# Performance work log

Measured on AMD Instinct MI355X. Metric: run time of the kernel, lower is better.

The kernel has to match this reference:

```python
import jax, jax.numpy as jnp
import numpy as np
from jax import lax

B, CX, CZ, H, W = 8, 96, 96, 256, 256
HEADS = 4


def conv2d(x, w, groups=1, pad=0):
    return lax.conv_general_dilated(
        x, w, window_strides=(1, 1), padding=[(pad, pad), (pad, pad)],
        dimension_numbers=('NCHW', 'OIHW', 'NCHW'),
        feature_group_count=groups)


def setup_inputs() -> dict:
    key = jax.random.key(0)
    ks = jax.random.split(key, 8)
    def init_w(k, shape):
        fan_in = shape[1] * shape[2] * shape[3]
        bound = 1.0 / np.sqrt(fan_in)
        return jax.random.uniform(k, shape, jnp.float32, -bound, bound)
    return {
        'x': jax.random.normal(ks[0], (B, CX, H, W), jnp.float32),
        'z': jax.random.normal(ks[1], (B, CZ, H, W), jnp.float32),
        'kv_w1': init_w(ks[2], (2 * CZ, CZ, 1, 1)),
        'kv_w2': init_w(ks[3], (2 * CZ, 2, 3, 3)),   # grouped: groups=CZ, 2 in-ch per group
        'q_w1': init_w(ks[4], (CX, CX, 1, 1)),
        'q_w2': init_w(ks[5], (CX, 1, 3, 3)),        # depthwise: groups=CX
        'proj_w': init_w(ks[6], (CX, CX, 1, 1)),
        'temperature': jnp.ones((HEADS, 1, 1), jnp.float32),
    }


def _forward(x, z, kv_w1, kv_w2, q_w1, q_w2, proj_w, temperature):
    b, cx, h, w = x.shape
    cz = z.shape[1]
    hw = h * w
    kv = conv2d(conv2d(z, kv_w1), kv_w2, groups=cz, pad=1)   # [b, 2cz, h, w]
    q = conv2d(conv2d(x, q_w1), q_w2, groups=cx, pad=1)      # [b, cx, h, w]
    k, v = jnp.split(kv, 2, axis=1)
    # b (head c) h w -> b head c (h w)
    q = q.reshape(b, HEADS, cx // HEADS, hw)
    k = k.reshape(b, HEADS, cz // HEADS, hw)
    v = v.reshape(b, HEADS, cz // HEADS, hw)
    # L2 normalize along hw (torch F.normalize: x / max(||x||, eps))
    eps = 1e-12
    q = q / jnp.maximum(jnp.linalg.norm(q, axis=-1, keepdims=True), eps)
    k = k / jnp.maximum(jnp.linalg.norm(k, axis=-1, keepdims=True), eps)
    attn = jnp.einsum('bhcn,bhdn->bhcd', q, k) * temperature  # [b,head,cq,ck]
    attn = jax.nn.softmax(attn, axis=-1)
    out = jnp.einsum('bhcd,bhdn->bhcn', attn, v)              # [b,head,cq,hw]
    out = out.reshape(b, cx, h, w)
    return conv2d(out, proj_w)


def reference(x, z, kv_w1, kv_w2, q_w1, q_w2, proj_w, temperature):
    return _forward(x, z, kv_w1, kv_w2, q_w1, q_w2, proj_w, temperature)
```

## Files before the change

### kernel.cpp

```cpp
#include <hip/hip_runtime.h>
#include <math.h>

#define HWc 65536
#define Wd 256
#define Hd 256

typedef __attribute__((ext_vector_type(8))) short bf16x8;
typedef __attribute__((ext_vector_type(4))) float f32x4;

__device__ inline ushort f2bf_hi(float a) {
    uint u = __float_as_uint(a);
    uint r = u + 0x7FFFu + ((u >> 16) & 1u);
    return (ushort)(r >> 16);
}
__device__ inline float bf2f(ushort h) { return __uint_as_float((uint)h << 16); }

static const size_t SSQ_Q_OFF = 0;
static const size_t SSQ_K_OFF = 768;
static const size_t ATTN_OFF  = 1536;
static const size_t W2T_OFF   = 19968;
static const size_t KVW1T_OFF = 93696;
static const size_t QW1T_OFF  = 112128;
static const size_t WS1_OFF   = 121344;

__global__ void transpose_w_kernel(const float* __restrict__ w, float* __restrict__ wT,
                                   int O, int I) {
    int idx = blockIdx.x * 256 + threadIdx.x;
    if (idx < O * I) {
        int o = idx / I, c = idx % I;
        wT[(size_t)c * O + o] = w[idx];
    }
}

__global__ __launch_bounds__(384) void conv1x1_mfma(
    const float* __restrict__ in, const float* __restrict__ wT,
    int cstride, int woff, float* __restrict__ out)
{
    __shared__ ushort Ah[64][104];
    __shared__ ushort Al[64][104];
    int b = blockIdx.y;
    int px0 = blockIdx.x * 64;
    int t = threadIdx.x, lane = t & 63, wv = t >> 6;
    const float* inb = in + (size_t)b * 96 * HWc + px0;

    int m = 16 * wv + (lane & 15);
    int kbase = (lane >> 4) * 8;
    bf16x8 Bh[3], Bl[3];
#pragma unroll
    for (int ks = 0; ks < 3; ++ks) {
#pragma unroll
        for (int j = 0; j < 8; ++j) {
            int c = ks * 32 + kbase + j;
            float wval = wT[(size_t)c * cstride + woff + m];
            ushort hi = f2bf_hi(wval);
            float lo = wval - bf2f(hi);
            Bh[ks][j] = (short)hi;
            Bl[ks][j] = (short)f2bf_hi(lo);
        }
    }

#pragma unroll
    for (int rr = 0; rr < 4; ++rr) {
        int fi = rr * 384 + t;
        int c = fi >> 4;
        int p4 = (fi & 15) * 4;
        float4 v = *(const float4*)(inb + (size_t)c * HWc + p4);
        float vv[4] = {v.x, v.y, v.z, v.w};
#pragma unroll
        for (int e = 0; e < 4; ++e) {
            ushort hi = f2bf_hi(vv[e]);
            float lo = vv[e] - bf2f(hi);
            Ah[p4 + e][c] = hi;
            Al[p4 + e][c] = (ushort)f2bf_hi(lo);
        }
    }
    __syncthreads();

    f32x4 acc0 = {0.f, 0.f, 0.f, 0.f};
    f32x4 acc1 = {0.f, 0.f, 0.f, 0.f};
    f32x4 acc2 = {0.f, 0.f, 0.f, 0.f};
    f32x4 acc3 = {0.f, 0.f, 0.f, 0.f};
    int prow = lane & 15;

#pragma unroll
    for (int ks = 0; ks < 3; ++ks) {
        int ccol = ks * 32 + kbase;
#define DO_PT(PT, ACC)                                                         \
        {                                                                      \
            bf16x8 ah = *(const bf16x8*)&Ah[(PT) * 16 + prow][ccol];           \
            bf16x8 al = *(const bf16x8*)&Al[(PT) * 16 + prow][ccol];           \
            ACC = __builtin_amdgcn_mfma_f32_16x16x32_bf16(ah, Bh[ks], ACC, 0, 0, 0); \
            ACC = __builtin_amdgcn_mfma_f32_16x16x32_bf16(ah, Bl[ks], ACC, 0, 0, 0); \
            ACC = __builtin_amdgcn_mfma_f32_16x16x32_bf16(al, Bh[ks], ACC, 0, 0, 0); \
        }
        DO_PT(0, acc0) DO_PT(1, acc1) DO_PT(2, acc2) DO_PT(3, acc3)
#undef DO_PT
    }

    int pq = (lane >> 4) * 4;
    float* outm = out + (size_t)b * 96 * HWc + (size_t)m * HWc + px0 + pq;
    *(f32x4*)(outm + 0)  = acc0;
    *(f32x4*)(outm + 16) = acc1;
    *(f32x4*)(outm + 32) = acc2;
    *(f32x4*)(outm + 48) = acc3;
}

__global__ __launch_bounds__(256) void depthwise3x3_kernel(
    const float* __restrict__ in, const float* __restrict__ wq,
    float* __restrict__ out, float* __restrict__ ssq_q)
{
    __shared__ float red[4];
    int c = blockIdx.y, b = blockIdx.z;
    int t = threadIdx.x;
    int lane = t & 63;
    int xq = lane * 4;
    int yb = blockIdx.x * 32 + (t >> 6) * 8;

    const float* inc = in + ((size_t)(b * 96 + c)) * HWc;
    float* outc = out + ((size_t)(b * 96 + c)) * HWc;

    float w[9];
    const float* wp = wq + (size_t)c * 9;
#pragma unroll
    for (int i = 0; i < 9; ++i) w[i] = wp[i];

    float rows[3][6];

#define LOAD_ROW(yy, slot)                                                     \
    {                                                                          \
        float4 v_;                                                             \
        if ((unsigned)(yy) < (unsigned)Hd)                                     \
            v_ = *(const float4*)(inc + (size_t)(yy) * Wd + xq);               \
        else                                                                   \
            v_ = make_float4(0.f, 0.f, 0.f, 0.f);                              \
        float lw_ = __shfl_up(v_.w, 1, 64);                                    \
        float rx_ = __shfl_down(v_.x, 1, 64);                                  \
        rows[slot][0] = (lane > 0) ? lw_ : 0.f;                                \
        rows[slot][1] = v_.x; rows[slot][2] = v_.y;                            \
        rows[slot][3] = v_.z; rows[slot][4] = v_.w;                            \
        rows[slot][5] = (lane < 63) ? rx_ : 0.f;                               \
    }

    LOAD_ROW(yb - 1, 0);
    LOAD_ROW(yb, 1);

    float ssq = 0.f;
#pragma unroll
    for (int r = 0; r < 8; ++r) {
        LOAD_ROW(yb + r + 1, (r + 2) % 3);
        const float* ra = rows[r % 3];
        const float* rb = rows[(r + 1) % 3];
        const float* rc = rows[(r + 2) % 3];
        float a[4] = {0.f, 0.f, 0.f, 0.f};
#pragma unroll
        for (int dx = 0; dx < 3; ++dx)
#pragma unroll
            for (int px = 0; px < 4; ++px) {
                a[px] = fmaf(w[dx],     ra[px + dx], a[px]);
                a[px] = fmaf(w[3 + dx], rb[px + dx], a[px]);
                a[px] = fmaf(w[6 + dx], rc[px + dx], a[px]);
            }
        *(float4*)(outc + (size_t)(yb + r) * Wd + xq) = *(float4*)a;
#pragma unroll
        for (int px = 0; px < 4; ++px) ssq = fmaf(a[px], a[px], ssq);
    }
#undef LOAD_ROW

#pragma unroll
    for (int off = 32; off; off >>= 1) ssq += __shfl_down(ssq, off, 64);
    int wvi = t >> 6;
    if (lane == 0) red[wvi] = ssq;
    __syncthreads();
    if (t == 0) atomicAdd(&ssq_q[b * 96 + c], red[0] + red[1] + red[2] + red[3]);
}

#define CONV_PAIR(P, SS0, SS1)                                                 \
    {                                                                          \
        const float* m0 = midb + (size_t)(2 * (P)) * HWc;                      \
        const float* m1 = m0 + HWc;                                            \
        const float* wp_ = &wls[(P) * 36];                                     \
        float k0[4] = {0.f, 0.f, 0.f, 0.f};                                    \
        float k1[4] = {0.f, 0.f, 0.f, 0.f};                                    \
        _Pragma("unroll")                                                      \
        for (int dy = 0; dy < 3; ++dy) {                                       \
            int yy = y + dy - 1;                                               \
            if ((unsigned)yy < (unsigned)Hd) {                                 \
                _Pragma("unroll")                                              \
                for (int ic = 0; ic < 2; ++ic) {                               \
                    const float* base = (ic ? m1 : m0) + (size_t)yy * Wd;      \
                    float4 cv = *(const float4*)(base + x0);                   \
                    float rr[6];                                               \
                    rr[0] = (x0 > 0) ? base[x0 - 1] : 0.f;                     \
                    rr[1] = cv.x; rr[2] = cv.y; rr[3] = cv.z; rr[4] = cv.w;    \
                    rr[5] = (x0 < 252) ? base[x0 + 4] : 0.f;                   \
                    int wb_ = ic * 9 + dy * 3;                                 \
                    _Pragma("unroll")                                          \
                    for (int px = 0; px < 4; ++px) {                           \
                        _Pragma("unroll")                                      \
                        for (int dx = 0; dx < 3; ++dx) {                       \
                            k0[px] = fmaf(wp_[wb_ + dx],      rr[px + dx], k0[px]); \
                            k1[px] = fmaf(wp_[18 + wb_ + dx], rr[px + dx], k1[px]); \
                        }                                                      \
                    }                                                          \
                }                                                              \
            }                                                                  \
        }                                                                      \
        _Pragma("unroll")                                                      \
        for (int px = 0; px < 4; ++px) {                                       \
            SS0 = fmaf(k0[px], k0[px], SS0);                                   \
            SS1 = fmaf(k1[px], k1[px], SS1);                                   \
        }                                                                      \
        *(float4*)&ks[2 * (P)][l32 * 4]     = *(float4*)k0;                    \
        *(float4*)&ks[2 * (P) + 1][l32 * 4] = *(float4*)k1;                    \
    }

__global__ __launch_bounds__(256) void k_logits_kernel(
    const float* __restrict__ mid, const float* __restrict__ w2,
    const float* __restrict__ qg, float* __restrict__ attn_raw,
    float* __restrict__ ssq_k)
{
    __shared__ float qs[24][132];
    __shared__ float ks[24][132];
    __shared__ float wls[24 * 18];

    int bx = blockIdx.x;
    int yt = bx >> 1, xh = bx & 1;
    int h = blockIdx.y, b = blockIdx.z;
    int xbase = xh * 128;
    int t = threadIdx.x, lane = t & 63, wvi = t >> 6;
    int hi = lane >> 5, l32 = lane & 31;
    int i0 = (lane >> 3) * 3, j0 = (lane & 7) * 3;

    const float* midb = mid + ((size_t)b * 96 + h * 24) * HWc;
    const float* qb   = qg  + ((size_t)b * 96 + h * 24) * HWc;

    if (t < 108)
        *(float4*)&wls[4 * t] = *(const float4*)(w2 + (size_t)h * 432 + 4 * t);

    int pA = 2 * wvi + hi;
    int pB = 8 + 2 * wvi + hi;
    int x0 = xbase + l32 * 4;

    float acc[3][3];
#pragma unroll
    for (int a = 0; a < 3; ++a)
#pragma unroll
        for (int c2 = 0; c2 < 3; ++c2) acc[a][c2] = 0.f;
    float ssqA0 = 0.f, ssqA1 = 0.f, ssqB0 = 0.f, ssqB1 = 0.f;

    __syncthreads();

    for (int r = 0; r < 8; ++r) {
        int y = yt * 8 + r;
        __syncthreads();

        {
            const float* qrow = qb + (size_t)y * Wd + xbase;
            int fi = t;
            *(float4*)&qs[fi >> 5][(fi & 31) * 4] =
                *(const float4*)(qrow + (size_t)(fi >> 5) * HWc + (fi & 31) * 4);
            fi = t + 256;
            *(float4*)&qs[fi >> 5][(fi & 31) * 4] =
                *(const float4*)(qrow + (size_t)(fi >> 5) * HWc + (fi & 31) * 4);
        }
        CONV_PAIR(pA, ssqA0, ssqA1);
        if (t < 128) {
            CONV_PAIR(pB, ssqB0, ssqB1);
        } else {
            const float* qrow = qb + (size_t)y * Wd + xbase;
            int fi = 512 + (t - 128);
            *(float4*)&qs[fi >> 5][(fi & 31) * 4] =
                *(const float4*)(qrow + (size_t)(fi >> 5) * HWc + (fi & 31) * 4);
            fi = 640 + (t - 128);
            *(float4*)&qs[fi >> 5][(fi & 31) * 4] =
                *(const float4*)(qrow + (size_t)(fi >> 5) * HWc + (fi & 31) * 4);
        }
        __syncthreads();

        int n0 = wvi * 32;
#pragma unroll 4
        for (int nn = 0; nn < 8; ++nn) {
            int n = n0 + nn * 4;
            float4 q0v = *(const float4*)&qs[i0][n];
            float4 q1v = *(const float4*)&qs[i0 + 1][n];
            float4 q2v = *(const float4*)&qs[i0 + 2][n];
            float4 k0v = *(const float4*)&ks[j0][n];
            float4 k1v = *(const float4*)&ks[j0 + 1][n];
            float4 k2v = *(const float4*)&ks[j0 + 2][n];
            acc[0][0] += q0v.x*k0v.x + q0v.y*k0v.y + q0v.z*k0v.z + q0v.w*k0v.w;
            acc[0][1] += q0v.x*k1v.x + q0v.y*k1v.y + q0v.z*k1v.z + q0v.w*k1v.w;
            acc[0][2] += q0v.x*k2v.x + q0v.y*k2v.y + q0v.z*k2v.z + q0v.w*k2v.w;
            acc[1][0] += q1v.x*k0v.x + q1v.y*k0v.y + q1v.z*k0v.z + q1v.w*k0v.w;
            acc[1][1] += q1v.x*k1v.x + q1v.y*k1v.y + q1v.z*k1v.z + q1v.w*k1v.w;
            acc[1][2] += q1v.x*k2v.x + q1v.y*k2v.y + q1v.z*k2v.z + q1v.w*k2v.w;
            acc[2][0] += q2v.x*k0v.x + q2v.y*k0v.y + q2v.z*k0v.z + q2v.w*k0v.w;
            acc[2][1] += q2v.x*k1v.x + q2v.y*k1v.y + q2v.z*k1v.z + q2v.w*k1v.w;
            acc[2][2] += q2v.x*k2v.x + q2v.y*k2v.y + q2v.z*k2v.z + q2v.w*k2v.w;
        }
    }

    {
        float s0 = ssqA0, s1 = ssqA1;
#pragma unroll
        for (int off = 16; off; off >>= 1) {
            s0 += __shfl_down(s0, off, 32);
            s1 += __shfl_down(s1, off, 32);
        }
        if (l32 == 0) {
            atomicAdd(&ssq_k[b * 96 + h * 24 + 2 * pA],     s0);
            atomicAdd(&ssq_k[b * 96 + h * 24 + 2 * pA + 1], s1);
        }
    }
    if (t < 128) {
        float s0 = ssqB0, s1 = ssqB1;
#pragma unroll
        for (int off = 16; off; off >>= 1) {
            s0 += __shfl_down(s0, off, 32);
            s1 += __shfl_down(s1, off, 32);
        }
        if (l32 == 0) {
            atomicAdd(&ssq_k[b * 96 + h * 24 + 2 * pB],     s0);
            atomicAdd(&ssq_k[b * 96 + h * 24 + 2 * pB + 1], s1);
        }
    }

    __syncthreads();
    float* redbuf = &qs[0][0];
#pragma unroll
    for (int a = 0; a < 3; ++a)
#pragma unroll
        for (int c2 = 0; c2 < 3; ++c2)
            redbuf[wvi * 576 + (i0 + a) * 24 + (j0 + c2)] = acc[a][c2];
    __syncthreads();
    for (int p_ = t; p_ < 576; p_ += 256) {
        float s4 = redbuf[p_] + redbuf[576 + p_] + redbuf[1152 + p_] + redbuf[1728 + p_];
        atomicAdd(&attn_raw[((size_t)b * 4 + h) * 576 + p_], s4);
    }
}

__global__ __launch_bounds__(256) void softmax_fold_kernel(
    const float* __restrict__ attn_raw,
    const float* __restrict__ ssq_q, const float* __restrict__ ssq_k,
    const float* __restrict__ temp, const float* __restrict__ projw,
    float* __restrict__ W2T)
{
    __shared__ float s[24][25];
    __shared__ float rq[24], rk[24];
    int h = blockIdx.x, b = blockIdx.y;
    int t = threadIdx.x;

    if (t < 24) {
        rq[t] = 1.f / fmaxf(sqrtf(ssq_q[b * 96 + h * 24 + t]), 1e-12f);
        rk[t] = 1.f / fmaxf(sqrtf(ssq_k[b * 96 + h * 24 + t]), 1e-12f);
    }
    __syncthreads();
    float T = temp[h];
    for (int p = t; p < 576; p += 256) {
        int i = p / 24, j = p % 24;
        s[i][j] = attn_raw[(size_t)(b * 4 + h) * 576 + p] * T * rq[i] * rk[j];
    }
    __syncthreads();
    if (t < 24) {
        float m = -1e30f;
#pragma unroll
        for (int j = 0; j < 24; ++j) m = fmaxf(m, s[t][j]);
        float sum = 0.f;
#pragma unroll
        for (int j = 0; j < 24; ++j) { float e = __expf(s[t][j] - m); s[t][j] = e; sum += e; }
        float inv = 1.f / sum;
#pragma unroll
        for (int j = 0; j < 24; ++j) s[t][j] *= inv;
    }
    __syncthreads();
    for (int m_ = t; m_ < 96 * 24; m_ += 256) {
        int d = m_ % 24, co = m_ / 24;
        float acc = 0.f;
#pragma unroll
        for (int c = 0; c < 24; ++c)
            acc += projw[co * 96 + h * 24 + c] * s[c][d];
        W2T[(size_t)b * 9216 + (size_t)(h * 24 + d) * 96 + co] = acc;
    }
}

__global__ __launch_bounds__(256) void v_proj_kernel(
    const float* __restrict__ mid, const float* __restrict__ w2,
    const float* __restrict__ W2T, float* __restrict__ out)
{
    __shared__ float v_lds[48][128];
    __shared__ float wls[48 * 36];

    int bx = blockIdx.x, b = blockIdx.y;
    int y0 = (bx >> 1) * 2;
    int x0 = (bx & 1) * 128;
    int t = threadIdx.x;
    const float* midb = mid + (size_t)b * 96 * HWc;

    {
        const float* vw = w2 + 96 * 18;
        for (int i = t; i < 432; i += 256)
            *(float4*)&wls[4 * i] = *(const float4*)(vw + 4 * i);
    }

    int x = t & 127;
    int mh = __builtin_amdgcn_readfirstlane(t >> 7);
    const float* wb2 = W2T + (size_t)b * 9216 + mh * 48;

    int s4 = (t & 31) * 4;
    int xg = x0 + s4;

#pragma unroll 1
    for (int r = 0; r < 2; ++r) {
        int y = y0 + r;
        float acc[48];
#pragma unroll
        for (int m = 0; m < 48; ++m) acc[m] = 0.f;

#pragma unroll 1
        for (int cc = 0; cc < 2; ++cc) {
            __syncthreads();
#pragma unroll
            for (int j = 0; j < 3; ++j) {
                int pair = cc * 24 + j * 8 + (t >> 5);
                const float* m0 = midb + (size_t)(2 * pair) * HWc;
                const float* m1 = m0 + HWc;
                const float* wp_ = &wls[pair * 36];
                float k0[4] = {0.f, 0.f, 0.f, 0.f};
                float k1[4] = {0.f, 0.f, 0.f, 0.f};
#pragma unroll
                for (int dy = 0; dy < 3; ++dy) {
                    int yy = y + dy - 1;
                    if ((unsigned)yy < (unsigned)Hd) {
#pragma unroll
                        for (int ic = 0; ic < 2; ++ic) {
                            const float* base = (ic ? m1 : m0) + (size_t)yy * Wd;
                            float4 cv = *(const float4*)(base + xg);
                            float rr[6];
                            rr[0] = (xg > 0) ? base[xg - 1] : 0.f;
                            rr[1] = cv.x; rr[2] = cv.y; rr[3] = cv.z; rr[4] = cv.w;
                            rr[5] = (xg < 252) ? base[xg + 4] : 0.f;
                            int wb_ = ic * 9 + dy * 3;
#pragma unroll
                            for (int px = 0; px < 4; ++px) {
#pragma unroll
                                for (int dx = 0; dx < 3; ++dx) {
                                    k0[px] = fmaf(wp_[wb_ + dx],      rr[px + dx], k0[px]);
                                    k1[px] = fmaf(wp_[18 + wb_ + dx], rr[px + dx], k1[px]);
                                }
                            }
                        }
                    }
                }
                int lc = 2 * (j * 8 + (t >> 5));
                *(float4*)&v_lds[lc][s4]     = *(float4*)k0;
                *(float4*)&v_lds[lc + 1][s4] = *(float4*)k1;
            }
            __syncthreads();
#pragma unroll 4
            for (int cl = 0; cl < 48; ++cl) {
                float v = v_lds[cl][x];
                const float* wc = wb2 + (size_t)(cc * 48 + cl) * 96;
#pragma unroll
                for (int m = 0; m < 48; ++m) acc[m] = fmaf(wc[m], v, acc[m]);
            }
        }

        float* outb = out + (size_t)b * 96 * HWc + (size_t)(mh * 48) * HWc
                    + (size_t)y * Wd + x0 + x;
#pragma unroll
        for (int m = 0; m < 48; ++m) outb[(size_t)m * HWc] = acc[m];
    }
}

extern "C" void kernel_launch(void* const* d_in, const int* in_sizes, int n_in,
                              void* d_out, int out_size, void* d_ws, size_t ws_size,
                              hipStream_t stream) {
    const float* x     = (const float*)d_in[0];
    const float* z     = (const float*)d_in[1];
    const float* kvw1  = (const float*)d_in[2];
    const float* kvw2  = (const float*)d_in[3];
    const float* qw1   = (const float*)d_in[4];
    const float* qw2   = (const float*)d_in[5];
    const float* projw = (const float*)d_in[6];
    const float* temp  = (const float*)d_in[7];
    float* out = (float*)d_out;
    float* ws  = (float*)d_ws;
    (void)in_sizes; (void)n_in; (void)out_size; (void)ws_size;

    float* ssq_q = ws + SSQ_Q_OFF;
    float* ssq_k = ws + SSQ_K_OFF;
    float* attn  = ws + ATTN_OFF;
    float* W2T   = ws + W2T_OFF;
    float* kvw1T = ws + KVW1T_OFF;
    float* qw1T  = ws + QW1T_OFF;
    float* ws1   = ws + WS1_OFF;

    hipMemsetAsync(ws, 0, (768 + 768 + 18432) * sizeof(float), stream);

    transpose_w_kernel<<<dim3(72), 256, 0, stream>>>(kvw1, kvw1T, 192, 96);
    transpose_w_kernel<<<dim3(36), 256, 0, stream>>>(qw1, qw1T, 96, 96);

    conv1x1_mfma<<<dim3(1024, 8), 384, 0, stream>>>(x, qw1T, 96, 0, ws1);
    depthwise3x3_kernel<<<dim3(8, 96, 8), 256, 0, stream>>>(ws1, qw2, out, ssq_q);

    conv1x1_mfma<<<dim3(1024, 8), 384, 0, stream>>>(z, kvw1T, 192, 0, ws1);
    k_logits_kernel<<<dim3(64, 4, 8), 256, 0, stream>>>(ws1, kvw2, out, attn, ssq_k);

    softmax_fold_kernel<<<dim3(4, 8), 256, 0, stream>>>(attn, ssq_q, ssq_k, temp, projw, W2T);

    conv1x1_mfma<<<dim3(1024, 8), 384, 0, stream>>>(z, kvw1T, 192, 96, ws1);
    v_proj_kernel<<<dim3(256, 8), 256, 0, stream>>>(ws1, kvw2, W2T, out);
}
```

Baseline: 777.1 us.

## Move fused V-conv and projection to split-bf16 MFMA, prepack weight fragments

The final stage, a grouped 3x3 on V followed by the folded attention-times-projection matrix, now stages the V tile into swizzled LDS as hi/lo bf16 pairs. It then does the 96x96 channel mix with bf16 MFMA using three products per pair to keep near-fp32 accuracy, replacing the scalar FMA loop over 48 register accumulators. The 1x1 conv weights and the folded W2 are pre-split into hi/lo bf16 fragments in a prep kernel, so each conv block loads vectors instead of converting weights per element. The trade-off is smaller blocks with redundant halo loads for the 3x3, plus a small precision change from the bf16 split.

```diff
diff --git a/kernel.cpp b/kernel.cpp
--- a/kernel.cpp
+++ b/kernel.cpp
@@ -18,23 +18,28 @@
 static const size_t SSQ_Q_OFF = 0;
 static const size_t SSQ_K_OFF = 768;
 static const size_t ATTN_OFF  = 1536;
-static const size_t W2T_OFF   = 19968;
-static const size_t KVW1T_OFF = 93696;
-static const size_t QW1T_OFF  = 112128;
+static const size_t QWF_OFF   = 19968;
+static const size_t KWF_OFF   = 29184;
+static const size_t VWF_OFF   = 38400;
+static const size_t W2F_OFF   = 47616;
 static const size_t WS1_OFF   = 121344;
 
-__global__ void transpose_w_kernel(const float* __restrict__ w, float* __restrict__ wT,
-                                   int O, int I) {
+__global__ void prep_wfrag(const float* __restrict__ w, int woff,
+                           ushort* __restrict__ wf) {
     int idx = blockIdx.x * 256 + threadIdx.x;
-    if (idx < O * I) {
-        int o = idx / I, c = idx % I;
-        wT[(size_t)c * O + o] = w[idx];
+    if (idx < 9216) {
+        int m = idx / 96, c = idx % 96;
+        float val = w[(size_t)(woff + m) * 96 + c];
+        ushort hi = f2bf_hi(val);
+        float lo = val - bf2f(hi);
+        wf[(c >> 5) * 3072 + m * 32 + (c & 31)] = hi;
+        wf[9216 + (c >> 5) * 3072 + m * 32 + (c & 31)] = f2bf_hi(lo);
     }
 }
 
 __global__ __launch_bounds__(384) void conv1x1_mfma(
-    const float* __restrict__ in, const float* __restrict__ wT,
-    int cstride, int woff, float* __restrict__ out)
+    const float* __restrict__ in, const ushort* __restrict__ wf,
+    float* __restrict__ out)
 {
     __shared__ ushort Ah[64][104];
     __shared__ ushort Al[64][104];
@@ -48,15 +53,8 @@
     bf16x8 Bh[3], Bl[3];
 #pragma unroll
     for (int ks = 0; ks < 3; ++ks) {
-#pragma unroll
-        for (int j = 0; j < 8; ++j) {
-            int c = ks * 32 + kbase + j;
-            float wval = wT[(size_t)c * cstride + woff + m];
-            ushort hi = f2bf_hi(wval);
-            float lo = wval - bf2f(hi);
-            Bh[ks][j] = (short)hi;
-            Bl[ks][j] = (short)f2bf_hi(lo);
-        }
+        Bh[ks] = *(const bf16x8*)&wf[ks * 3072 + m * 32 + kbase];
+        Bl[ks] = *(const bf16x8*)&wf[9216 + ks * 3072 + m * 32 + kbase];
     }
 
 #pragma unroll
@@ -342,7 +340,7 @@
     const float* __restrict__ attn_raw,
     const float* __restrict__ ssq_q, const float* __restrict__ ssq_k,
     const float* __restrict__ temp, const float* __restrict__ projw,
-    float* __restrict__ W2T)
+    ushort* __restrict__ W2F)
 {
     __shared__ float s[24][25];
     __shared__ float rq[24], rk[24];
@@ -372,103 +370,131 @@
         for (int j = 0; j < 24; ++j) s[t][j] *= inv;
     }
     __syncthreads();
+    ushort* wfb = W2F + (size_t)b * 18432;
     for (int m_ = t; m_ < 96 * 24; m_ += 256) {
         int d = m_ % 24, co = m_ / 24;
         float acc = 0.f;
 #pragma unroll
         for (int c = 0; c < 24; ++c)
             acc += projw[co * 96 + h * 24 + c] * s[c][d];
-        W2T[(size_t)b * 9216 + (size_t)(h * 24 + d) * 96 + co] = acc;
-    }
-}
-
-__global__ __launch_bounds__(256) void v_proj_kernel(
+        int dv = h * 24 + d;
+        int ks = dv >> 5, kk = dv & 31;
+        ushort hi = f2bf_hi(acc);
+        float lo = acc - bf2f(hi);
+        wfb[ks * 3072 + co * 32 + kk] = hi;
+        wfb[9216 + ks * 3072 + co * 32 + kk] = f2bf_hi(lo);
+    }
+}
+
+__global__ __launch_bounds__(384) void v_proj_mfma(
     const float* __restrict__ mid, const float* __restrict__ w2,
-    const float* __restrict__ W2T, float* __restrict__ out)
+    const ushort* __restrict__ W2F, float* __restrict__ out)
 {
-    __shared__ float v_lds[48][128];
-    __shared__ float wls[48 * 36];
+    __shared__ ushort Ah[64][128];
+    __shared__ ushort Al[64][128];
+    __shared__ float wls[1728];
 
     int bx = blockIdx.x, b = blockIdx.y;
-    int y0 = (bx >> 1) * 2;
-    int x0 = (bx & 1) * 128;
-    int t = threadIdx.x;
+    int y = bx >> 2;
+    int x0 = (bx & 3) * 64;
+    int t = threadIdx.x, lane = t & 63, wv = t >> 6;
     const float* midb = mid + (size_t)b * 96 * HWc;
 
+    for (int i = t; i < 432; i += 384)
+        *(float4*)&wls[4 * i] = *(const float4*)(w2 + 96 * 18 + 4 * i);
+
+    int m = 16 * wv + (lane & 15);
+    int kbase = (lane >> 4) * 8;
+    const ushort* wfb = W2F + (size_t)b * 18432;
+    bf16x8 Bh[3], Bl[3];
+#pragma unroll
+    for (int ks = 0; ks < 3; ++ks) {
+        Bh[ks] = *(const bf16x8*)&wfb[ks * 3072 + m * 32 + kbase];
+        Bl[ks] = *(const bf16x8*)&wfb[9216 + ks * 3072 + m * 32 + kbase];
+    }
+    __syncthreads();
+
     {
-        const float* vw = w2 + 96 * 18;
-        for (int i = t; i < 432; i += 256)
-            *(float4*)&wls[4 * i] = *(const float4*)(vw + 4 * i);
-    }
-
-    int x = t & 127;
-    int mh = __builtin_amdgcn_readfirstlane(t >> 7);
-    const float* wb2 = W2T + (size_t)b * 9216 + mh * 48;
-
-    int s4 = (t & 31) * 4;
-    int xg = x0 + s4;
-
-#pragma unroll 1
-    for (int r = 0; r < 2; ++r) {
-        int y = y0 + r;
-        float acc[48];
-#pragma unroll
-        for (int m = 0; m < 48; ++m) acc[m] = 0.f;
-
-#pragma unroll 1
-        for (int cc = 0; cc < 2; ++cc) {
-            __syncthreads();
-#pragma unroll
-            for (int j = 0; j < 3; ++j) {
-                int pair = cc * 24 + j * 8 + (t >> 5);
-                const float* m0 = midb + (size_t)(2 * pair) * HWc;
-                const float* m1 = m0 + HWc;
-                const float* wp_ = &wls[pair * 36];
-                float k0[4] = {0.f, 0.f, 0.f, 0.f};
-                float k1[4] = {0.f, 0.f, 0.f, 0.f};
-#pragma unroll
-                for (int dy = 0; dy < 3; ++dy) {
-                    int yy = y + dy - 1;
-                    if ((unsigned)yy < (unsigned)Hd) {
-#pragma unroll
-                        for (int ic = 0; ic < 2; ++ic) {
-                            const float* base = (ic ? m1 : m0) + (size_t)yy * Wd;
-                            float4 cv = *(const float4*)(base + xg);
-                            float rr[6];
-                            rr[0] = (xg > 0) ? base[xg - 1] : 0.f;
-                            rr[1] = cv.x; rr[2] = cv.y; rr[3] = cv.z; rr[4] = cv.w;
-                            rr[5] = (xg < 252) ? base[xg + 4] : 0.f;
-                            int wb_ = ic * 9 + dy * 3;
-#pragma unroll
-                            for (int px = 0; px < 4; ++px) {
-#pragma unroll
-                                for (int dx = 0; dx < 3; ++dx) {
-                                    k0[px] = fmaf(wp_[wb_ + dx],      rr[px + dx], k0[px]);
-                                    k1[px] = fmaf(wp_[18 + wb_ + dx], rr[px + dx], k1[px]);
-                                }
-                            }
+        int p = t >> 3;
+        int xl = (t & 7) * 8;
+        int xg = x0 + xl;
+        const float* m0 = midb + (size_t)(2 * p) * HWc;
+        const float* m1 = m0 + HWc;
+        const float* wp_ = &wls[p * 36];
+        float k0[8] = {0.f,0.f,0.f,0.f,0.f,0.f,0.f,0.f};
+        float k1[8] = {0.f,0.f,0.f,0.f,0.f,0.f,0.f,0.f};
+#pragma unroll
+        for (int dy = 0; dy < 3; ++dy) {
+            int yy = y + dy - 1;
+            if ((unsigned)yy < (unsigned)Hd) {
+#pragma unroll
+                for (int ic = 0; ic < 2; ++ic) {
+                    const float* base = (ic ? m1 : m0) + (size_t)yy * Wd;
+                    float4 a = *(const float4*)(base + xg);
+                    float4 b2 = *(const float4*)(base + xg + 4);
+                    float rr[10];
+                    rr[0] = (xg > 0) ? base[xg - 1] : 0.f;
+                    rr[1] = a.x; rr[2] = a.y; rr[3] = a.z; rr[4] = a.w;
+                    rr[5] = b2.x; rr[6] = b2.y; rr[7] = b2.z; rr[8] = b2.w;
+                    rr[9] = (xg + 8 < 256) ? base[xg + 8] : 0.f;
+                    int wb_ = ic * 9 + dy * 3;
+#pragma unroll
+                    for (int px = 0; px < 8; ++px) {
+#pragma unroll
+                        for (int dx = 0; dx < 3; ++dx) {
+                            k0[px] = fmaf(wp_[wb_ + dx],      rr[px + dx], k0[px]);
+                            k1[px] = fmaf(wp_[18 + wb_ + dx], rr[px + dx], k1[px]);
                         }
                     }
                 }
-                int lc = 2 * (j * 8 + (t >> 5));
-                *(float4*)&v_lds[lc][s4]     = *(float4*)k0;
-                *(float4*)&v_lds[lc + 1][s4] = *(float4*)k1;
             }
-            __syncthreads();
-#pragma unroll 4
-            for (int cl = 0; cl < 48; ++cl) {
-                float v = v_lds[cl][x];
-                const float* wc = wb2 + (size_t)(cc * 48 + cl) * 96;
-#pragma unroll
-                for (int m = 0; m < 48; ++m) acc[m] = fmaf(wc[m], v, acc[m]);
-            }
-        }
-
-        float* outb = out + (size_t)b * 96 * HWc + (size_t)(mh * 48) * HWc
-                    + (size_t)y * Wd + x0 + x;
-#pragma unroll
-        for (int m = 0; m < 48; ++m) outb[(size_t)m * HWc] = acc[m];
-    }
+        }
+#pragma unroll
+        for (int px = 0; px < 8; ++px) {
+            int row = xl + px;
+            uint sw = (uint)(row & 7) << 4;
+            uint off = ((uint)(4 * p)) ^ sw;
+            ushort h0 = f2bf_hi(k0[px]);
+            ushort h1 = f2bf_hi(k1[px]);
+            float l0 = k0[px] - bf2f(h0);
+            float l1 = k1[px] - bf2f(h1);
+            *(uint*)((char*)&Ah[row][0] + off) = (uint)h0 | ((uint)h1 << 16);
+            *(uint*)((char*)&Al[row][0] + off) =
+                (uint)f2bf_hi(l0) | ((uint)f2bf_hi(l1) << 16);
+        }
+    }
+    __syncthreads();
+
+    f32x4 acc0 = {0.f, 0.f, 0.f, 0.f};
+    f32x4 acc1 = {0.f, 0.f, 0.f, 0.f};
+    f32x4 acc2 = {0.f, 0.f, 0.f, 0.f};
+    f32x4 acc3 = {0.f, 0.f, 0.f, 0.f};
+    int prow = lane & 15;
+
+#pragma unroll
+    for (int ks = 0; ks < 3; ++ks) {
+        uint cbyte = (uint)(ks * 32 + kbase) * 2;
+#define DO_PT(PT, ACC)                                                         \
+        {                                                                      \
+            int row = (PT) * 16 + prow;                                        \
+            uint sw = (uint)(row & 7) << 4;                                    \
+            bf16x8 ah = *(const bf16x8*)((char*)&Ah[row][0] + (cbyte ^ sw));   \
+            bf16x8 al = *(const bf16x8*)((char*)&Al[row][0] + (cbyte ^ sw));   \
+            ACC = __builtin_amdgcn_mfma_f32_16x16x32_bf16(ah, Bh[ks], ACC, 0, 0, 0); \
+            ACC = __builtin_amdgcn_mfma_f32_16x16x32_bf16(ah, Bl[ks], ACC, 0, 0, 0); \
+            ACC = __builtin_amdgcn_mfma_f32_16x16x32_bf16(al, Bh[ks], ACC, 0, 0, 0); \
+        }
+        DO_PT(0, acc0) DO_PT(1, acc1) DO_PT(2, acc2) DO_PT(3, acc3)
+#undef DO_PT
+    }
+
+    int pq = (lane >> 4) * 4;
+    float* outm = out + (size_t)b * 96 * HWc + (size_t)m * HWc
+                + (size_t)y * Wd + x0 + pq;
+    *(f32x4*)(outm + 0)  = acc0;
+    *(f32x4*)(outm + 16) = acc1;
+    *(f32x4*)(outm + 32) = acc2;
+    *(f32x4*)(outm + 48) = acc3;
 }
 
 extern "C" void kernel_launch(void* const* d_in, const int* in_sizes, int n_in,
@@ -489,24 +515,26 @@
     float* ssq_q = ws + SSQ_Q_OFF;
     float* ssq_k = ws + SSQ_K_OFF;
     float* attn  = ws + ATTN_OFF;
-    float* W2T   = ws + W2T_OFF;
-    float* kvw1T = ws + KVW1T_OFF;
-    float* qw1T  = ws + QW1T_OFF;
+    ushort* qwf  = (ushort*)(ws + QWF_OFF);
+    ushort* kwf  = (ushort*)(ws + KWF_OFF);
+    ushort* vwf  = (ushort*)(ws + VWF_OFF);
+    ushort* w2f  = (ushort*)(ws + W2F_OFF);
     float* ws1   = ws + WS1_OFF;
 
     hipMemsetAsync(ws, 0, (768 + 768 + 18432) * sizeof(float), stream);
 
-    transpose_w_kernel<<<dim3(72), 256, 0, stream>>>(kvw1, kvw1T, 192, 96);
-    transpose_w_kernel<<<dim3(36), 256, 0, stream>>>(qw1, qw1T, 96, 96);
-
-    conv1x1_mfma<<<dim3(1024, 8), 384, 0, stream>>>(x, qw1T, 96, 0, ws1);
+    prep_wfrag<<<dim3(36), 256, 0, stream>>>(qw1, 0, qwf);
+    prep_wfrag<<<dim3(36), 256, 0, stream>>>(kvw1, 0, kwf);
+    prep_wfrag<<<dim3(36), 256, 0, stream>>>(kvw1, 96, vwf);
+
+    conv1x1_mfma<<<dim3(1024, 8), 384, 0, stream>>>(x, qwf, ws1);
     depthwise3x3_kernel<<<dim3(8, 96, 8), 256, 0, stream>>>(ws1, qw2, out, ssq_q);
 
-    conv1x1_mfma<<<dim3(1024, 8), 384, 0, stream>>>(z, kvw1T, 192, 0, ws1);
+    conv1x1_mfma<<<dim3(1024, 8), 384, 0, stream>>>(z, kwf, ws1);
     k_logits_kernel<<<dim3(64, 4, 8), 256, 0, stream>>>(ws1, kvw2, out, attn, ssq_k);
 
-    softmax_fold_kernel<<<dim3(4, 8), 256, 0, stream>>>(attn, ssq_q, ssq_k, temp, projw, W2T);
-
-    conv1x1_mfma<<<dim3(1024, 8), 384, 0, stream>>>(z, kvw1T, 192, 96, ws1);
-    v_proj_kernel<<<dim3(256, 8), 256, 0, stream>>>(ws1, kvw2, W2T, out);
-}
+    softmax_fold_kernel<<<dim3(4, 8), 256, 0, stream>>>(attn, ssq_q, ssq_k, temp, projw, w2f);
+
+    conv1x1_mfma<<<dim3(1024, 8), 384, 0, stream>>>(z, vwf, ws1);
+    v_proj_mfma<<<dim3(1024, 8), 384, 0, stream>>>(ws1, kvw2, w2f, out);
+}
```

New measurement: 737.8 us (median of 2 runs). -5.1%, faster.
